# Optimization experiments

Hardware: AMD Instinct MI355X
Metric: run time of the kernel (lower is better)

The kernel has to match this reference:

```python
import jax, jax.numpy as jnp
import numpy as np

G = 512          # graphs per batch
NPG = 90         # nodes per graph (AAL-90 atlas)
N = G * NPG      # 46080 total nodes
DEG = 20
E = N * DEG      # 921600 edges
F_IN = 90
H = 64           # hidden_channels (args.hc)
K = 70           # sort-pool k


def setup_inputs() -> dict:
    key = jax.random.key(0)
    ks = jax.random.split(key, 14)
    x = jax.random.normal(ks[0], (N, F_IN), dtype=jnp.float32)
    # edges kept within each graph (realistic PyG batching)
    gid = jax.random.randint(ks[1], (E,), 0, G)
    src = gid * NPG + jax.random.randint(ks[2], (E,), 0, NPG)
    dst = gid * NPG + jax.random.randint(ks[3], (E,), 0, NPG)
    edge_index = jnp.stack([src, dst]).astype(jnp.int64)
    batch = (jnp.arange(N) // NPG).astype(jnp.int64)
    s_in = 1.0 / np.sqrt(F_IN)
    s_h = 1.0 / np.sqrt(H)
    s_p = 1.0 / np.sqrt(H * K)
    # SAGEConv: out = mean_aggr(x_j) @ W_l + x_i @ W_r + b
    W1l = jax.random.uniform(ks[4], (F_IN, H), jnp.float32, -s_in, s_in)
    W1r = jax.random.uniform(ks[5], (F_IN, H), jnp.float32, -s_in, s_in)
    b1 = jnp.zeros((H,), jnp.float32)
    W2l = jax.random.uniform(ks[6], (H, H), jnp.float32, -s_h, s_h)
    W2r = jax.random.uniform(ks[7], (H, H), jnp.float32, -s_h, s_h)
    b2 = jnp.zeros((H,), jnp.float32)
    Wl1 = jax.random.uniform(ks[8], (H * K, H), jnp.float32, -s_p, s_p)
    bl1 = jax.random.uniform(ks[9], (H,), jnp.float32, -s_p, s_p)
    Wl2 = jax.random.uniform(ks[10], (H, 1), jnp.float32, -s_h, s_h)
    bl2 = jax.random.uniform(ks[11], (1,), jnp.float32, -s_h, s_h)
    return {"x": x, "edge_index": edge_index, "batch": batch,
            "W1l": W1l, "W1r": W1r, "b1": b1,
            "W2l": W2l, "W2r": W2r, "b2": b2,
            "Wl1": Wl1, "bl1": bl1, "Wl2": Wl2, "bl2": bl2}


def sage_conv(x, src, dst, Wl, Wr, b):
    # gather source features, scatter-mean to destinations
    msg = x[src]                                              # [E, F]
    s = jax.ops.segment_sum(msg, dst, num_segments=N)         # [N, F]
    cnt = jax.ops.segment_sum(jnp.ones((src.shape[0], 1), x.dtype),
                              dst, num_segments=N)            # [N, 1]
    mean = s / jnp.maximum(cnt, 1.0)
    return mean @ Wl + x @ Wr + b


def global_sort_pool(x, k):
    # nodes per graph are contiguous and fixed (NPG >= k, no padding needed)
    xr = x.reshape(G, NPG, H)
    order = jnp.argsort(-xr[:, :, -1], axis=1)[:, :k]          # sort by last channel, desc
    top = jnp.take_along_axis(xr, order[:, :, None], axis=1)   # [G, k, H]
    return top.reshape(G, k * H)


def reference(x, edge_index, batch, W1l, W1r, b1, W2l, W2r, b2, Wl1, bl1, Wl2, bl2):
    src, dst = edge_index[0], edge_index[1]
    h = sage_conv(x, src, dst, W1l, W1r, b1)       # conv1
    x_train = h
    h = jax.nn.relu(h)
    h = sage_conv(h, src, dst, W2l, W2r, b2)       # conv2
    p = global_sort_pool(h, K)                     # [G, K*H]
    # dropout is identity at eval time
    p = p @ Wl1 + bl1
    p = p @ Wl2 + bl2
    out = jnp.squeeze(jax.nn.sigmoid(p))           # [G]
    return out, x_train
```

## Files before the change

### kernel.cpp

```cpp
#include <hip/hip_runtime.h>

typedef unsigned short u16;
typedef unsigned int u32;
typedef unsigned char u8;
typedef unsigned long long u64;

#define GG   512
#define NPG  90
#define NTOT (GG*NPG)
#define NED  921600
#define FIN  90
#define HC   64
#define KP   70
#define AW   23
#define AWG  (NPG*AW)

#define SAD  92
#define SP   68
#define APW  25

#define WF_W1L 0
#define WF_W1R 5760
#define WF_W2L 11520
#define WF_W2R 15616
#define WF_B1  19712
#define WF_B2  19776
#define WF_FOLD 19840
#define WF_ZC  24320
#define WF_FLAG 24321

__device__ __forceinline__ float bf2f(u16 u) {
    union { u32 i; float f; } v; v.i = ((u32)u) << 16; return v.f;
}
__device__ __forceinline__ float bflo(u32 u) {
    union { u32 i; float f; } v; v.i = u << 16; return v.f;
}
__device__ __forceinline__ float bfhi(u32 u) {
    union { u32 i; float f; } v; v.i = u & 0xFFFF0000u; return v.f;
}
__device__ __forceinline__ u16 f2bf(float f) {
    union { float f; u32 i; } v; v.f = f;
    u32 r = (v.i + 0x7FFFu + ((v.i >> 16) & 1u)) >> 16;
    return (u16)r;
}
__device__ __forceinline__ float ldadp(const void* p, long long i, int isf32) {
    return isf32 ? ((const float*)p)[i] : bf2f(((const u16*)p)[i]);
}

__global__ __launch_bounds__(256) void k_pre(
    const u32* __restrict__ xw, const int* __restrict__ ei,
    const void* W1l, const void* W1r, const void* b1,
    const void* W2l, const void* W2r, const void* b2,
    const void* Wl1, const void* bl1, const void* Wl2, const void* bl2,
    u32* __restrict__ A32, float* __restrict__ wf)
{
    __shared__ int sf;
    const int t = threadIdx.x;
    const int b = blockIdx.x;

    if (b < 900) {
        int lane = t & 63;
        u32 v = (lane < 16) ? (u32)ei[lane] : 0u;
        u64 bb = __ballot((lane & 1) && (v != 0));
        bool wide = (bb == 0ull);
        int e0 = b * 1024 + t * 4;
        int s[4], d[4];
        if (wide) {
            uint4 s01 = *(const uint4*)(ei + 2 * e0);
            uint4 s23 = *(const uint4*)(ei + 2 * e0 + 4);
            uint4 d01 = *(const uint4*)(ei + 2 * (NED + e0));
            uint4 d23 = *(const uint4*)(ei + 2 * (NED + e0) + 4);
            s[0] = (int)s01.x; s[1] = (int)s01.z; s[2] = (int)s23.x; s[3] = (int)s23.z;
            d[0] = (int)d01.x; d[1] = (int)d01.z; d[2] = (int)d23.x; d[3] = (int)d23.z;
        } else {
            uint4 ss = *(const uint4*)(ei + e0);
            uint4 dd = *(const uint4*)(ei + NED + e0);
            s[0] = (int)ss.x; s[1] = (int)ss.y; s[2] = (int)ss.z; s[3] = (int)ss.w;
            d[0] = (int)dd.x; d[1] = (int)dd.y; d[2] = (int)dd.z; d[3] = (int)dd.w;
        }
        #pragma unroll
        for (int k = 0; k < 4; ++k) {
            int dk = d[k];
            if ((unsigned)dk >= NTOT) continue;
            int g = (unsigned)dk / NPG;
            int dl = dk - g * NPG;
            int ls = s[k] - g * NPG;
            if ((unsigned)ls >= NPG) continue;
            atomicAdd(&A32[(size_t)g * AWG + dl * AW + (ls >> 2)],
                      1u << (8 * (ls & 3)));
        }
        return;
    }

    if (t < 64) {
        u32 e = (xw[t] >> 7) & 0xFF;
        u64 bb = __ballot(e >= 136);
        if (t == 0) sf = (bb != 0ull) ? 1 : 0;
    }
    __syncthreads();
    const int f32 = sf;

    if (b < 978) {
        int i = (b - 900) * 256 + t;
        if      (i < 5760)  wf[i] = ldadp(W1l, i, f32);
        else if (i < 11520) wf[i] = ldadp(W1r, i - 5760, f32);
        else if (i < 15616) wf[i] = ldadp(W2l, i - 11520, f32);
        else if (i < 19712) wf[i] = ldadp(W2r, i - 15616, f32);
        else if (i < 19776) wf[i] = ldadp(b1, i - 19712, f32);
        else if (i < 19840) wf[i] = ldadp(b2, i - 19776, f32);
        if (b == 900 && t == 0) wf[WF_FLAG] = f32 ? 1.0f : 0.0f;
    } else {
        int m = (b - 978) * 256 + t;
        if (m < 4480) {
            float s = 0.f;
            for (int j = 0; j < HC; ++j)
                s += ldadp(Wl1, (long long)m * HC + j, f32) * ldadp(Wl2, j, f32);
            wf[WF_FOLD + m] = s;
        } else if (m == 4480) {
            float s = ldadp(bl2, 0, f32);
            for (int j = 0; j < HC; ++j)
                s += ldadp(bl1, j, f32) * ldadp(Wl2, j, f32);
            wf[WF_ZC] = s;
        }
    }
}

__global__ __launch_bounds__(512, 4) void k_fused(
    const void* __restrict__ x, const u32* __restrict__ A32,
    const float* __restrict__ wf, void* __restrict__ dout)
{
    __shared__ __align__(16) char smem[67136];
    float* As    = (float*)smem;
    float* R1    = (float*)(smem + 33120);
    u32*   Apk   = (u32*)(smem + 57600);
    float* s_key = (float*)(smem + 66600);
    float* s_red = (float*)(smem + 66960);
    u16*   s_ord = (u16*)(smem + 66992);

    const int g = blockIdx.x;
    const int t = threadIdx.x;
    const bool isf32 = (wf[WF_FLAG] > 0.5f);

    const int l = t & 63;
    const int w = __builtin_amdgcn_readfirstlane(t >> 6);
    const int jb = w * 8;
    const int row0 = l;
    const bool has2 = (l < NPG - 64);
    const int row1 = has2 ? l + 64 : l;

    u32 abuf[5];
    {
        const u32* Ag = A32 + (size_t)g * AWG;
        #pragma unroll
        for (int j = 0; j < 5; ++j) {
            int p = t + j * 512;
            abuf[j] = (p < AWG) ? Ag[p] : 0u;
        }
    }

    if (isf32) {
        const float* xg = (const float*)x + (size_t)g * 8100;
        for (int p = t; p < 8100; p += 512) {
            int r = p / NPG, c = p - r * NPG;
            As[r * SAD + c] = xg[p];
        }
    } else {
        const u32* xg = (const u32*)((const u16*)x + (size_t)g * 8100);
        for (int p = t; p < 4050; p += 512) {
            int r = p / 45, c = (p - r * 45) * 2;
            u32 v = xg[p];
            As[r * SAD + c]     = bflo(v);
            As[r * SAD + c + 1] = bfhi(v);
        }
    }
    if (t < 180) As[(t >> 1) * SAD + 90 + (t & 1)] = 0.f;
    #pragma unroll
    for (int j = 0; j < 5; ++j) {
        int p = t + j * 512;
        if (p < AWG) {
            int r = p / AW, wc = p - r * AW;
            Apk[r * APW + wc] = abuf[j];
        }
    }
    __syncthreads();

    float accP[2][8], accQ[2][8];
    {
        const float* bb = wf + WF_B1 + jb;
        #pragma unroll
        for (int j = 0; j < 8; ++j) {
            float bv = bb[j];
            accP[0][j] = 0.f; accP[1][j] = 0.f;
            accQ[0][j] = bv;  accQ[1][j] = bv;
        }
    }
    {
        const float* WL = wf + WF_W1L + jb;
        const float* WR = wf + WF_W1R + jb;
        const float* X0 = As + row0 * SAD;
        const float* X1 = As + row1 * SAD;
        for (int k0 = 0; k0 < 23; ++k0) {
            float4 q0 = *(const float4*)(X0 + 4 * k0);
            float4 q1 = *(const float4*)(X1 + 4 * k0);
            float xa0[4] = {q0.x, q0.y, q0.z, q0.w};
            float xa1[4] = {q1.x, q1.y, q1.z, q1.w};
            #pragma unroll
            for (int jj = 0; jj < 4; ++jj) {
                int k = 4 * k0 + jj;
                float wl[8], wr[8];
                #pragma unroll
                for (int j = 0; j < 8; ++j) { wl[j] = WL[k * HC + j]; wr[j] = WR[k * HC + j]; }
                #pragma unroll
                for (int j = 0; j < 8; ++j) {
                    accP[0][j] += xa0[jj] * wl[j]; accQ[0][j] += xa0[jj] * wr[j];
                    accP[1][j] += xa1[jj] * wl[j]; accQ[1][j] += xa1[jj] * wr[j];
                }
            }
        }
    }
    __syncthreads();

    *(float4*)(R1 + row0 * SP + jb)     = make_float4(accP[0][0], accP[0][1], accP[0][2], accP[0][3]);
    *(float4*)(R1 + row0 * SP + jb + 4) = make_float4(accP[0][4], accP[0][5], accP[0][6], accP[0][7]);
    if (has2) {
        *(float4*)(R1 + row1 * SP + jb)     = make_float4(accP[1][0], accP[1][1], accP[1][2], accP[1][3]);
        *(float4*)(R1 + row1 * SP + jb + 4) = make_float4(accP[1][4], accP[1][5], accP[1][6], accP[1][7]);
    }
    __syncthreads();

    float r1v[2][8];
    float rc0, rc1;
    {
        float acc[2][8];
        float asum0 = 0.f, asum1 = 0.f;
        #pragma unroll
        for (int i = 0; i < 2; ++i)
            #pragma unroll
            for (int j = 0; j < 8; ++j) acc[i][j] = 0.f;
        const u32* A0 = Apk + row0 * APW;
        const u32* A1 = Apk + row1 * APW;
        for (int k0 = 0; k0 < 22; ++k0) {
            u32 w0 = A0[k0], w1 = A1[k0];
            #pragma unroll
            for (int jj = 0; jj < 4; ++jj) {
                int k = 4 * k0 + jj;
                float4 p0 = *(const float4*)(R1 + k * SP + jb);
                float4 p1 = *(const float4*)(R1 + k * SP + jb + 4);
                float pv[8] = {p0.x,p0.y,p0.z,p0.w,p1.x,p1.y,p1.z,p1.w};
                float a0 = (float)((w0 >> (8 * jj)) & 255u);
                float a1 = (float)((w1 >> (8 * jj)) & 255u);
                asum0 += a0; asum1 += a1;
                #pragma unroll
                for (int j = 0; j < 8; ++j) {
                    acc[0][j] += a0 * pv[j];
                    acc[1][j] += a1 * pv[j];
                }
            }
        }
        {
            u32 w0 = A0[22], w1 = A1[22];
            #pragma unroll
            for (int jj = 0; jj < 2; ++jj) {
                int k = 88 + jj;
                float4 p0 = *(const float4*)(R1 + k * SP + jb);
                float4 p1 = *(const float4*)(R1 + k * SP + jb + 4);
                float pv[8] = {p0.x,p0.y,p0.z,p0.w,p1.x,p1.y,p1.z,p1.w};
                float a0 = (float)((w0 >> (8 * jj)) & 255u);
                float a1 = (float)((w1 >> (8 * jj)) & 255u);
                asum0 += a0; asum1 += a1;
                #pragma unroll
                for (int j = 0; j < 8; ++j) {
                    acc[0][j] += a0 * pv[j];
                    acc[1][j] += a1 * pv[j];
                }
            }
        }
        rc0 = 1.0f / fmaxf(asum0, 1.0f);
        rc1 = 1.0f / fmaxf(asum1, 1.0f);
        #pragma unroll
        for (int i = 0; i < 2; ++i) {
            if (i == 0 || has2) {
                int n = i ? row1 : row0;
                float rc = i ? rc1 : rc0;
                float h[8];
                #pragma unroll
                for (int j = 0; j < 8; ++j) h[j] = fmaf(rc, acc[i][j], accQ[i][j]);
                size_t base = 512 + (size_t)(g * NPG + n) * HC + jb;
                if (isf32) {
                    *(float4*)((float*)dout + base)     = make_float4(h[0],h[1],h[2],h[3]);
                    *(float4*)((float*)dout + base + 4) = make_float4(h[4],h[5],h[6],h[7]);
                } else {
                    uint4 pk;
                    pk.x = (u32)f2bf(h[0]) | ((u32)f2bf(h[1]) << 16);
                    pk.y = (u32)f2bf(h[2]) | ((u32)f2bf(h[3]) << 16);
                    pk.z = (u32)f2bf(h[4]) | ((u32)f2bf(h[5]) << 16);
                    pk.w = (u32)f2bf(h[6]) | ((u32)f2bf(h[7]) << 16);
                    *(uint4*)((u16*)dout + base) = pk;
                }
                #pragma unroll
                for (int j = 0; j < 8; ++j) r1v[i][j] = fmaxf(h[j], 0.f);
            }
        }
    }
    __syncthreads();
    *(float4*)(R1 + row0 * SP + jb)     = make_float4(r1v[0][0], r1v[0][1], r1v[0][2], r1v[0][3]);
    *(float4*)(R1 + row0 * SP + jb + 4) = make_float4(r1v[0][4], r1v[0][5], r1v[0][6], r1v[0][7]);
    if (has2) {
        *(float4*)(R1 + row1 * SP + jb)     = make_float4(r1v[1][0], r1v[1][1], r1v[1][2], r1v[1][3]);
        *(float4*)(R1 + row1 * SP + jb + 4) = make_float4(r1v[1][4], r1v[1][5], r1v[1][6], r1v[1][7]);
    }
    __syncthreads();

    {
        const float* bb = wf + WF_B2 + jb;
        #pragma unroll
        for (int j = 0; j < 8; ++j) {
            float bv = bb[j];
            accP[0][j] = 0.f; accP[1][j] = 0.f;
            accQ[0][j] = bv;  accQ[1][j] = bv;
        }
    }
    {
        const float* WL = wf + WF_W2L + jb;
        const float* WR = wf + WF_W2R + jb;
        const float* V0 = R1 + row0 * SP;
        const float* V1 = R1 + row1 * SP;
        for (int k0 = 0; k0 < 16; ++k0) {
            float4 q0 = *(const float4*)(V0 + 4 * k0);
            float4 q1 = *(const float4*)(V1 + 4 * k0);
            float va0[4] = {q0.x, q0.y, q0.z, q0.w};
            float va1[4] = {q1.x, q1.y, q1.z, q1.w};
            #pragma unroll
            for (int jj = 0; jj < 4; ++jj) {
                int k = 4 * k0 + jj;
                float wl[8], wr[8];
                #pragma unroll
                for (int j = 0; j < 8; ++j) { wl[j] = WL[k * HC + j]; wr[j] = WR[k * HC + j]; }
                #pragma unroll
                for (int j = 0; j < 8; ++j) {
                    accP[0][j] += va0[jj] * wl[j]; accQ[0][j] += va0[jj] * wr[j];
                    accP[1][j] += va1[jj] * wl[j]; accQ[1][j] += va1[jj] * wr[j];
                }
            }
        }
    }
    __syncthreads();
    *(float4*)(R1 + row0 * SP + jb)     = make_float4(accP[0][0], accP[0][1], accP[0][2], accP[0][3]);
    *(float4*)(R1 + row0 * SP + jb + 4) = make_float4(accP[0][4], accP[0][5], accP[0][6], accP[0][7]);
    if (has2) {
        *(float4*)(R1 + row1 * SP + jb)     = make_float4(accP[1][0], accP[1][1], accP[1][2], accP[1][3]);
        *(float4*)(R1 + row1 * SP + jb + 4) = make_float4(accP[1][4], accP[1][5], accP[1][6], accP[1][7]);
    }
    __syncthreads();

    float h2v[2][8];
    {
        float acc[2][8];
        #pragma unroll
        for (int i = 0; i < 2; ++i)
            #pragma unroll
            for (int j = 0; j < 8; ++j) acc[i][j] = 0.f;
        const u32* A0 = Apk + row0 * APW;
        const u32* A1 = Apk + row1 * APW;
        for (int k0 = 0; k0 < 22; ++k0) {
            u32 w0 = A0[k0], w1 = A1[k0];
            #pragma unroll
            for (int jj = 0; jj < 4; ++jj) {
                int k = 4 * k0 + jj;
                float4 p0 = *(const float4*)(R1 + k * SP + jb);
                float4 p1 = *(const float4*)(R1 + k * SP + jb + 4);
                float pv[8] = {p0.x,p0.y,p0.z,p0.w,p1.x,p1.y,p1.z,p1.w};
                float a0 = (float)((w0 >> (8 * jj)) & 255u);
                float a1 = (float)((w1 >> (8 * jj)) & 255u);
                #pragma unroll
                for (int j = 0; j < 8; ++j) {
                    acc[0][j] += a0 * pv[j];
                    acc[1][j] += a1 * pv[j];
                }
            }
        }
        {
            u32 w0 = A0[22], w1 = A1[22];
            #pragma unroll
            for (int jj = 0; jj < 2; ++jj) {
                int k = 88 + jj;
                float4 p0 = *(const float4*)(R1 + k * SP + jb);
                float4 p1 = *(const float4*)(R1 + k * SP + jb + 4);
                float pv[8] = {p0.x,p0.y,p0.z,p0.w,p1.x,p1.y,p1.z,p1.w};
                float a0 = (float)((w0 >> (8 * jj)) & 255u);
                float a1 = (float)((w1 >> (8 * jj)) & 255u);
                #pragma unroll
                for (int j = 0; j < 8; ++j) {
                    acc[0][j] += a0 * pv[j];
                    acc[1][j] += a1 * pv[j];
                }
            }
        }
        #pragma unroll
        for (int i = 0; i < 2; ++i) {
            if (i == 0 || has2) {
                int n = i ? row1 : row0;
                float rc = i ? rc1 : rc0;
                #pragma unroll
                for (int j = 0; j < 8; ++j)
                    h2v[i][j] = fmaf(rc, acc[i][j], accQ[i][j]);
                if (w == 7) s_key[n] = h2v[i][7];
            }
        }
    }
    __syncthreads();
    *(float4*)(R1 + row0 * SP + jb)     = make_float4(h2v[0][0], h2v[0][1], h2v[0][2], h2v[0][3]);
    *(float4*)(R1 + row0 * SP + jb + 4) = make_float4(h2v[0][4], h2v[0][5], h2v[0][6], h2v[0][7]);
    if (has2) {
        *(float4*)(R1 + row1 * SP + jb)     = make_float4(h2v[1][0], h2v[1][1], h2v[1][2], h2v[1][3]);
        *(float4*)(R1 + row1 * SP + jb + 4) = make_float4(h2v[1][4], h2v[1][5], h2v[1][6], h2v[1][7]);
    }
    if (t < NPG) {
        float my = s_key[t];
        int r = 0;
        for (int m2 = 0; m2 < NPG; ++m2) {
            float km = s_key[m2];
            r += (km > my) || (km == my && m2 < t);
        }
        if (r < KP) s_ord[r] = (u16)t;
    }
    __syncthreads();

    float zp = 0.f;
    for (int p = t; p < KP * HC; p += 512) {
        int i = p >> 6, c = p & 63;
        int nn = s_ord[i];
        zp += R1[nn * SP + c] * wf[WF_FOLD + p];
    }
    #pragma unroll
    for (int off = 32; off > 0; off >>= 1) zp += __shfl_down(zp, off);
    if ((t & 63) == 0) s_red[t >> 6] = zp;
    __syncthreads();
    if (t == 0) {
        float z = wf[WF_ZC];
        #pragma unroll
        for (int i = 0; i < 8; ++i) z += s_red[i];
        float sg = 1.0f / (1.0f + expf(-z));
        if (isf32) ((float*)dout)[g] = sg;
        else       ((u16*)dout)[g]   = f2bf(sg);
    }
}

extern "C" void kernel_launch(void* const* d_in, const int* in_sizes, int n_in,
                              void* d_out, int out_size, void* d_ws, size_t ws_size,
                              hipStream_t stream) {
    const void* x   = d_in[0];
    const int*  ei  = (const int*)d_in[1];
    const void* W1l = d_in[3];
    const void* W1r = d_in[4];
    const void* b1  = d_in[5];
    const void* W2l = d_in[6];
    const void* W2r = d_in[7];
    const void* b2  = d_in[8];
    const void* Wl1 = d_in[9];
    const void* bl1 = d_in[10];
    const void* Wl2 = d_in[11];
    const void* bl2 = d_in[12];

    char* ws    = (char*)d_ws;
    u32*  A32   = (u32*)ws;
    float* wf   = (float*)(ws + 4239360);

    hipMemsetAsync(A32, 0, 4239360, stream);
    k_pre<<<996, 256, 0, stream>>>((const u32*)x, ei, W1l, W1r, b1, W2l, W2r, b2,
                                   Wl1, bl1, Wl2, bl2, A32, wf);
    k_fused<<<GG, 512, 0, stream>>>(x, A32, wf, d_out);
}
```

Before: 186.1 us.

## Merge preprocessing and fused GNN kernels into one persistent kernel with grid barriers

```diff
diff --git a/kernel.cpp b/kernel.cpp
--- a/kernel.cpp
+++ b/kernel.cpp
@@ -9,6 +9,7 @@
 #define NPG  90
 #define NTOT (GG*NPG)
 #define NED  921600
+#define EPB  1800
 #define FIN  90
 #define HC   64
 #define KP   70
@@ -27,7 +28,7 @@
 #define WF_B2  19776
 #define WF_FOLD 19840
 #define WF_ZC  24320
-#define WF_FLAG 24321
+#define WF_BAR 24321
 
 __device__ __forceinline__ float bf2f(u16 u) {
     union { u32 i; float f; } v; v.i = ((u32)u) << 16; return v.f;
@@ -47,87 +48,25 @@
     return isf32 ? ((const float*)p)[i] : bf2f(((const u16*)p)[i]);
 }
 
-__global__ __launch_bounds__(256) void k_pre(
-    const u32* __restrict__ xw, const int* __restrict__ ei,
+__device__ __forceinline__ void gridbar(u32* bar, u32 target) {
+    __threadfence();
+    __syncthreads();
+    if (threadIdx.x == 0) {
+        __hip_atomic_fetch_add(bar, 1u, __ATOMIC_ACQ_REL, __HIP_MEMORY_SCOPE_AGENT);
+        while (__hip_atomic_load(bar, __ATOMIC_ACQUIRE, __HIP_MEMORY_SCOPE_AGENT) < target)
+            __builtin_amdgcn_s_sleep(8);
+    }
+    __syncthreads();
+    __threadfence();
+}
+
+__global__ __launch_bounds__(512, 4) void k_mega(
+    const void* __restrict__ x, const int* __restrict__ ei,
     const void* W1l, const void* W1r, const void* b1,
     const void* W2l, const void* W2r, const void* b2,
     const void* Wl1, const void* bl1, const void* Wl2, const void* bl2,
-    u32* __restrict__ A32, float* __restrict__ wf)
-{
-    __shared__ int sf;
-    const int t = threadIdx.x;
-    const int b = blockIdx.x;
-
-    if (b < 900) {
-        int lane = t & 63;
-        u32 v = (lane < 16) ? (u32)ei[lane] : 0u;
-        u64 bb = __ballot((lane & 1) && (v != 0));
-        bool wide = (bb == 0ull);
-        int e0 = b * 1024 + t * 4;
-        int s[4], d[4];
-        if (wide) {
-            uint4 s01 = *(const uint4*)(ei + 2 * e0);
-            uint4 s23 = *(const uint4*)(ei + 2 * e0 + 4);
-            uint4 d01 = *(const uint4*)(ei + 2 * (NED + e0));
-            uint4 d23 = *(const uint4*)(ei + 2 * (NED + e0) + 4);
-            s[0] = (int)s01.x; s[1] = (int)s01.z; s[2] = (int)s23.x; s[3] = (int)s23.z;
-            d[0] = (int)d01.x; d[1] = (int)d01.z; d[2] = (int)d23.x; d[3] = (int)d23.z;
-        } else {
-            uint4 ss = *(const uint4*)(ei + e0);
-            uint4 dd = *(const uint4*)(ei + NED + e0);
-            s[0] = (int)ss.x; s[1] = (int)ss.y; s[2] = (int)ss.z; s[3] = (int)ss.w;
-            d[0] = (int)dd.x; d[1] = (int)dd.y; d[2] = (int)dd.z; d[3] = (int)dd.w;
-        }
-        #pragma unroll
-        for (int k = 0; k < 4; ++k) {
-            int dk = d[k];
-            if ((unsigned)dk >= NTOT) continue;
-            int g = (unsigned)dk / NPG;
-            int dl = dk - g * NPG;
-            int ls = s[k] - g * NPG;
-            if ((unsigned)ls >= NPG) continue;
-            atomicAdd(&A32[(size_t)g * AWG + dl * AW + (ls >> 2)],
-                      1u << (8 * (ls & 3)));
-        }
-        return;
-    }
-
-    if (t < 64) {
-        u32 e = (xw[t] >> 7) & 0xFF;
-        u64 bb = __ballot(e >= 136);
-        if (t == 0) sf = (bb != 0ull) ? 1 : 0;
-    }
-    __syncthreads();
-    const int f32 = sf;
-
-    if (b < 978) {
-        int i = (b - 900) * 256 + t;
-        if      (i < 5760)  wf[i] = ldadp(W1l, i, f32);
-        else if (i < 11520) wf[i] = ldadp(W1r, i - 5760, f32);
-        else if (i < 15616) wf[i] = ldadp(W2l, i - 11520, f32);
-        else if (i < 19712) wf[i] = ldadp(W2r, i - 15616, f32);
-        else if (i < 19776) wf[i] = ldadp(b1, i - 19712, f32);
-        else if (i < 19840) wf[i] = ldadp(b2, i - 19776, f32);
-        if (b == 900 && t == 0) wf[WF_FLAG] = f32 ? 1.0f : 0.0f;
-    } else {
-        int m = (b - 978) * 256 + t;
-        if (m < 4480) {
-            float s = 0.f;
-            for (int j = 0; j < HC; ++j)
-                s += ldadp(Wl1, (long long)m * HC + j, f32) * ldadp(Wl2, j, f32);
-            wf[WF_FOLD + m] = s;
-        } else if (m == 4480) {
-            float s = ldadp(bl2, 0, f32);
-            for (int j = 0; j < HC; ++j)
-                s += ldadp(bl1, j, f32) * ldadp(Wl2, j, f32);
-            wf[WF_ZC] = s;
-        }
-    }
-}
-
-__global__ __launch_bounds__(512, 4) void k_fused(
-    const void* __restrict__ x, const u32* __restrict__ A32,
-    const float* __restrict__ wf, void* __restrict__ dout)
+    u32* __restrict__ A32, float* __restrict__ wf, u32* __restrict__ bar,
+    void* __restrict__ dout)
 {
     __shared__ __align__(16) char smem[67136];
     float* As    = (float*)smem;
@@ -139,8 +78,6 @@
 
     const int g = blockIdx.x;
     const int t = threadIdx.x;
-    const bool isf32 = (wf[WF_FLAG] > 0.5f);
-
     const int l = t & 63;
     const int w = __builtin_amdgcn_readfirstlane(t >> 6);
     const int jb = w * 8;
@@ -148,14 +85,17 @@
     const bool has2 = (l < NPG - 64);
     const int row1 = has2 ? l + 64 : l;
 
-    u32 abuf[5];
-    {
-        const u32* Ag = A32 + (size_t)g * AWG;
-        #pragma unroll
-        for (int j = 0; j < 5; ++j) {
-            int p = t + j * 512;
-            abuf[j] = (p < AWG) ? Ag[p] : 0u;
-        }
+    bool isf32;
+    {
+        u32 v = ((const u32*)x)[l];
+        u32 e = (v >> 7) & 0xFF;
+        u64 bb = __ballot(e >= 136);
+        isf32 = (bb != 0ull);
+    }
+
+    {
+        u32* Az = A32 + (size_t)g * AWG;
+        for (int p = t; p < AWG; p += 512) Az[p] = 0u;
     }
 
     if (isf32) {
@@ -174,15 +114,71 @@
         }
     }
     if (t < 180) As[(t >> 1) * SAD + 90 + (t & 1)] = 0.f;
-    #pragma unroll
-    for (int j = 0; j < 5; ++j) {
-        int p = t + j * 512;
-        if (p < AWG) {
-            int r = p / AW, wc = p - r * AW;
-            Apk[r * APW + wc] = abuf[j];
-        }
-    }
-    __syncthreads();
+
+    if (g < 39) {
+        int i = g * 512 + t;
+        if (i < 19840) {
+            if      (i < 5760)  wf[i] = ldadp(W1l, i, isf32);
+            else if (i < 11520) wf[i] = ldadp(W1r, i - 5760, isf32);
+            else if (i < 15616) wf[i] = ldadp(W2l, i - 11520, isf32);
+            else if (i < 19712) wf[i] = ldadp(W2r, i - 15616, isf32);
+            else if (i < 19776) wf[i] = ldadp(b1, i - 19712, isf32);
+            else                wf[i] = ldadp(b2, i - 19776, isf32);
+        }
+    } else if (g < 48) {
+        int m = (g - 39) * 512 + t;
+        if (m < 4480) {
+            float s = 0.f;
+            for (int j = 0; j < HC; ++j)
+                s += ldadp(Wl1, (long long)m * HC + j, isf32) * ldadp(Wl2, j, isf32);
+            wf[WF_FOLD + m] = s;
+        } else if (m == 4480) {
+            float s = ldadp(bl2, 0, isf32);
+            for (int j = 0; j < HC; ++j)
+                s += ldadp(bl1, j, isf32) * ldadp(Wl2, j, isf32);
+            wf[WF_ZC] = s;
+        }
+    }
+
+    gridbar(bar, GG);
+
+    {
+        u32 v = (l < 16) ? (u32)ei[l] : 0u;
+        u64 bb = __ballot((l & 1) && (v != 0));
+        bool wide = (bb == 0ull);
+        const int ebase = g * EPB;
+        if (wide) {
+            for (int p = t; p < EPB; p += 512) {
+                int e = ebase + p;
+                int s = ei[2 * e];
+                int d = ei[2 * (NED + e)];
+                unsigned dk = (unsigned)d;
+                if (dk < NTOT) {
+                    int gg = (int)(dk / NPG);
+                    int dl = (int)dk - gg * NPG;
+                    int ls = s - gg * NPG;
+                    if ((unsigned)ls < NPG)
+                        atomicAdd(&A32[(size_t)gg * AWG + dl * AW + (ls >> 2)],
+                                  1u << (8 * (ls & 3)));
+                }
+            }
+        } else {
+            for (int p = t; p < EPB; p += 512) {
+                int e = ebase + p;
+                int s = ei[e];
+                int d = ei[NED + e];
+                unsigned dk = (unsigned)d;
+                if (dk < NTOT) {
+                    int gg = (int)(dk / NPG);
+                    int dl = (int)dk - gg * NPG;
+                    int ls = s - gg * NPG;
+                    if ((unsigned)ls < NPG)
+                        atomicAdd(&A32[(size_t)gg * AWG + dl * AW + (ls >> 2)],
+                                  1u << (8 * (ls & 3)));
+                }
+            }
+        }
+    }
 
     float accP[2][8], accQ[2][8];
     {
@@ -218,8 +214,26 @@
             }
         }
     }
-    __syncthreads();
-
+
+    gridbar(bar, 2 * GG);
+
+    {
+        const u32* Ag = A32 + (size_t)g * AWG;
+        u32 abuf[5];
+        #pragma unroll
+        for (int j = 0; j < 5; ++j) {
+            int p = t + j * 512;
+            abuf[j] = (p < AWG) ? Ag[p] : 0u;
+        }
+        #pragma unroll
+        for (int j = 0; j < 5; ++j) {
+            int p = t + j * 512;
+            if (p < AWG) {
+                int r = p / AW, wc = p - r * AW;
+                Apk[r * APW + wc] = abuf[j];
+            }
+        }
+    }
     *(float4*)(R1 + row0 * SP + jb)     = make_float4(accP[0][0], accP[0][1], accP[0][2], accP[0][3]);
     *(float4*)(R1 + row0 * SP + jb + 4) = make_float4(accP[0][4], accP[0][5], accP[0][6], accP[0][7]);
     if (has2) {
@@ -465,9 +479,9 @@
     char* ws    = (char*)d_ws;
     u32*  A32   = (u32*)ws;
     float* wf   = (float*)(ws + 4239360);
-
-    hipMemsetAsync(A32, 0, 4239360, stream);
-    k_pre<<<996, 256, 0, stream>>>((const u32*)x, ei, W1l, W1r, b1, W2l, W2r, b2,
-                                   Wl1, bl1, Wl2, bl2, A32, wf);
-    k_fused<<<GG, 512, 0, stream>>>(x, A32, wf, d_out);
-}
+    u32*  bar   = (u32*)(wf + WF_BAR);
+
+    hipMemsetAsync(bar, 0, 4, stream);
+    k_mega<<<GG, 512, 0, stream>>>(x, ei, W1l, W1r, b1, W2l, W2r, b2,
+                                   Wl1, bl1, Wl2, bl2, A32, wf, bar, d_out);
+}
```

New measurement: 696.8 us. 3.74x slower.
